# Performance work log

Measured on AMD Instinct MI355X. Metric: run time of the kernel, lower is better.

Reference implementation:

```python
import jax, jax.numpy as jnp
import numpy as np

# --- static configuration (mirrors PMETorchPME(alpha=1.0, mesh=1.0), interpolation_nodes=6) ---
ALPHA = 1.0            # Gaussian smearing sigma of CoulombPotential
MESH_SPACING = 1.0
BOX_L = 120.0
NS = (120, 120, 120)   # ceil(BOX_L / MESH_SPACING) per axis; static for jit
ORDER = 6              # interpolation nodes (6-point stencil per axis)
N_ATOMS = 100000
PI = np.pi


def _interp_weights(x):
    # x: (N,3) offsets in [-0.5, 0.5) relative to the midpoint of the 6-point stencil.
    # Lagrange interpolation on nodes t_j = j - 2.5, j = 0..5 (even-order, midpoint-centered).
    t = np.arange(ORDER) - (ORDER - 1) / 2.0                 # (6,) node positions
    diff = x[..., None] - jnp.asarray(t, x.dtype)            # (N,3,6)
    ws = []
    for j in range(ORDER):
        idx = [k for k in range(ORDER) if k != j]
        denom = float(np.prod([t[j] - t[k] for k in idx]))
        ws.append(jnp.prod(diff[..., idx], axis=-1) / denom)
    return jnp.stack(ws, axis=-1)                            # (N,3,6)


def _stencil(coords, box):
    # Map positions to mesh units, build per-particle 6x6x6 stencil weights + flat mesh indices.
    frac = coords @ jnp.linalg.inv(box)                      # fractional coordinates
    pos = frac * jnp.asarray(NS, coords.dtype)               # (N,3) in mesh units
    i0 = jnp.floor(pos)
    x = pos - (i0 + 0.5)                                     # offset from stencil midpoint
    w = _interp_weights(x)                                   # (N,3,6)
    offs = jnp.arange(ORDER, dtype=jnp.int32) - (ORDER // 2 - 1)   # [-2..3]
    ns_i = jnp.asarray(NS, jnp.int32)
    g = (i0.astype(jnp.int32)[..., None] + offs) % ns_i[None, :, None]  # (N,3,6) periodic
    W = w[:, 0, :, None, None] * w[:, 1, None, :, None] * w[:, 2, None, None, :]   # (N,6,6,6)
    flat = (g[:, 0, :, None, None] * NS[1] + g[:, 1, None, :, None]) * NS[2] + g[:, 2, None, None, :]
    n = coords.shape[0]
    return W.reshape(n, -1), flat.reshape(n, -1)             # (N,216) each


def _kspace_kernel(box, dtype):
    # G(k) = 4*pi * exp(-sigma^2 k^2 / 2) / k^2, zero at k=0 (CoulombPotential.lr_from_k_sq)
    inv_cell = jnp.linalg.inv(box)
    m0 = jnp.fft.fftfreq(NS[0]) * NS[0]
    m1 = jnp.fft.fftfreq(NS[1]) * NS[1]
    m2 = jnp.fft.rfftfreq(NS[2]) * NS[2]
    m = jnp.stack(jnp.meshgrid(m0, m1, m2, indexing="ij"), axis=-1).astype(dtype)
    k = 2.0 * PI * jnp.einsum("xyzm,nm->xyzn", m, inv_cell)  # k = 2*pi * inv(cell) @ m
    k_sq = jnp.sum(k * k, axis=-1)
    safe = jnp.where(k_sq > 0, k_sq, 1.0)
    return jnp.where(k_sq > 0, 4.0 * PI * jnp.exp(-0.5 * ALPHA * ALPHA * k_sq) / safe, 0.0)


def setup_inputs() -> dict:
    key = jax.random.key(0)
    k1, k2 = jax.random.split(key)
    coords = jax.random.uniform(k1, (N_ATOMS, 3), dtype=jnp.float32) * BOX_L
    box = (BOX_L * jnp.eye(3, dtype=jnp.float32))
    charges = jax.random.normal(k2, (N_ATOMS, 1), dtype=jnp.float32)
    return {"coords": coords, "box": box, "charges": charges}


def reference(coords, box, charges):
    q = charges[:, 0]                                        # (N,)
    W, flat = _stencil(coords, box)                          # (N,216)
    ntot = NS[0] * NS[1] * NS[2]
    # charge spreading (scatter-add)
    mesh = jnp.zeros((ntot,), coords.dtype).at[flat.reshape(-1)].add((W * q[:, None]).reshape(-1))
    mesh = mesh.reshape(NS)
    # FFT convolution with the reciprocal-space Coulomb kernel
    G = _kspace_kernel(box, coords.dtype)
    pot_mesh = jnp.fft.irfftn(jnp.fft.rfftn(mesh, norm="backward") * G, s=NS, norm="forward")
    # gather back to particles
    pot = jnp.sum(pot_mesh.reshape(-1)[flat] * W, axis=-1)   # (N,)
    volume = jnp.abs(jnp.linalg.det(box))
    pot = pot / volume
    pot = pot - q * (np.sqrt(2.0 / PI) / ALPHA)              # remove self-contribution
    pot = pot - 2.0 * (PI * ALPHA * ALPHA) * jnp.sum(q) / volume  # charge-neutral background
    pot = pot / 2.0
    return jnp.sum(q * pot)                                  # energy = sum(charges * potentials)
```

## Files before the change

kernel.cpp:

```cpp
#include <hip/hip_runtime.h>
#include <math.h>

#define NMESH 120
#define NKZ 61
#define ALPHA_C 1.0

#define TILE 12
#define NTPD 10
#define NTILE 1000
#define FP 17
#define ZPAD 20
#define FPSTRIDE 5792
#define CAP 256

#define CHUNK 128
#define WXA_OFF 0
#define WYA_OFF (CHUNK*ZPAD)
#define WZA_OFF (2*CHUNK*ZPAD)
#define LYS_OFF (3*CHUNK*ZPAD)
#define SMEMF   (LYS_OFF + CHUNK)

#define YCH 12
#define XCH 4
#define YROW 137

#define NSLOT 64
#define SLOTSTRIDE 8
#define W120C (-0.052359877559829887f)

typedef float v2f __attribute__((ext_vector_type(2)));

#define EK_OFF      0
#define Q_OFF       4096
#define Q2_OFF      8192
#define COUNTS_OFF  12288
#define BUF_OFF     115264
#define C1_OFF      23283264
#define C2_OFF      115264
#define SORTED_OFF  (C1_OFF + 4096)

__device__ inline void inv3(const float* b, float* ib) {
    float a00=b[0],a01=b[1],a02=b[2],a10=b[3],a11=b[4],a12=b[5],a20=b[6],a21=b[7],a22=b[8];
    float c00 =  a11*a22 - a12*a21;
    float c01 = -(a10*a22 - a12*a20);
    float c02 =  a10*a21 - a11*a20;
    float c10 = -(a01*a22 - a02*a21);
    float c11 =  a00*a22 - a02*a20;
    float c12 = -(a00*a21 - a01*a20);
    float c20 =  a01*a12 - a02*a11;
    float c21 = -(a00*a12 - a02*a10);
    float c22 =  a00*a11 - a01*a10;
    float det = a00*c00 + a01*c01 + a02*c02;
    float inv = 1.0f/det;
    ib[0]=c00*inv; ib[1]=c10*inv; ib[2]=c20*inv;
    ib[3]=c01*inv; ib[4]=c11*inv; ib[5]=c21*inv;
    ib[6]=c02*inv; ib[7]=c12*inv; ib[8]=c22*inv;
}

__device__ inline void atom_pos(const float* __restrict__ box, float c0, float c1, float c2,
                                float* p) {
    float ib[9]; inv3(box, ib);
    #pragma unroll
    for (int d=0; d<3; ++d)
        p[d] = (c0*ib[0+d] + c1*ib[3+d] + c2*ib[6+d]) * 120.0f;
}

__device__ inline int wrap120(int i) { return ((i % 120) + 120) % 120; }

__device__ inline void lag6(float x, float* w) {
    float df[6];
    #pragma unroll
    for (int k=0;k<6;++k) df[k] = x - ((float)k - 2.5f);
    w[0] = df[1]*df[2]*df[3]*df[4]*df[5] * (-1.0f/120.0f);
    w[1] = df[0]*df[2]*df[3]*df[4]*df[5] * ( 1.0f/24.0f);
    w[2] = df[0]*df[1]*df[3]*df[4]*df[5] * (-1.0f/12.0f);
    w[3] = df[0]*df[1]*df[2]*df[4]*df[5] * ( 1.0f/12.0f);
    w[4] = df[0]*df[1]*df[2]*df[3]*df[5] * (-1.0f/24.0f);
    w[5] = df[0]*df[1]*df[2]*df[3]*df[4] * ( 1.0f/120.0f);
}

__device__ inline int halo_pairs(int c, int* t, int* l) {
    int r = c % 12, ti = c / 12, n = 0;
    t[n] = ti;          l[n] = r + 2;  n++;
    if (r < 3)  { t[n] = (ti+9)%10; l[n] = r + 14; n++; }
    if (r >= 10){ t[n] = (ti+1)%10; l[n] = r - 10; n++; }
    return n;
}

__device__ inline void dft8(const float2* xin, float2* Y) {
    const float S = 0.70710678118654752f;
    float2 a=xin[0], b=xin[2], c=xin[4], d=xin[6];
    float s02r=a.x+c.x, s02i=a.y+c.y, d02r=a.x-c.x, d02i=a.y-c.y;
    float s13r=b.x+d.x, s13i=b.y+d.y, d13r=b.x-d.x, d13i=b.y-d.y;
    float2 E0 = make_float2(s02r+s13r, s02i+s13i);
    float2 E1 = make_float2(d02r+d13i, d02i-d13r);
    float2 E2 = make_float2(s02r-s13r, s02i-s13i);
    float2 E3 = make_float2(d02r-d13i, d02i+d13r);
    a=xin[1]; b=xin[3]; c=xin[5]; d=xin[7];
    s02r=a.x+c.x; s02i=a.y+c.y; d02r=a.x-c.x; d02i=a.y-c.y;
    s13r=b.x+d.x; s13i=b.y+d.y; d13r=b.x-d.x; d13i=b.y-d.y;
    float2 O0 = make_float2(s02r+s13r, s02i+s13i);
    float2 O1 = make_float2(d02r+d13i, d02i-d13r);
    float2 O2 = make_float2(s02r-s13r, s02i-s13i);
    float2 O3 = make_float2(d02r-d13i, d02i+d13r);
    float t1r = S*(O1.x + O1.y), t1i = S*(O1.y - O1.x);
    float t2r = O2.y,            t2i = -O2.x;
    float t3r = S*(O3.y - O3.x), t3i = -S*(O3.x + O3.y);
    Y[0] = make_float2(E0.x + O0.x, E0.y + O0.y);
    Y[4] = make_float2(E0.x - O0.x, E0.y - O0.y);
    Y[1] = make_float2(E1.x + t1r,  E1.y + t1i);
    Y[5] = make_float2(E1.x - t1r,  E1.y - t1i);
    Y[2] = make_float2(E2.x + t2r,  E2.y + t2i);
    Y[6] = make_float2(E2.x - t2r,  E2.y - t2i);
    Y[3] = make_float2(E3.x + t3r,  E3.y + t3i);
    Y[7] = make_float2(E3.x - t3r,  E3.y - t3i);
}

__global__ void scatter_q_kernel(const float* __restrict__ coords,
                                 const float* __restrict__ box,
                                 const float* __restrict__ charges,
                                 int* __restrict__ counts,
                                 float4* __restrict__ sorted,
                                 double* __restrict__ qslots,
                                 double* __restrict__ q2slots, int n) {
    int i = blockIdx.x*blockDim.x + threadIdx.x;
    float v = 0.f, v2 = 0.f;
    if (i < n) {
        float p[3]; atom_pos(box, coords[3*i], coords[3*i+1], coords[3*i+2], p);
        float q = charges[i];
        v = q; v2 = q*q;
        int t[3];
        #pragma unroll
        for (int d=0; d<3; ++d) t[d] = wrap120((int)floorf(p[d])) / TILE;
        int tile = (t[0]*NTPD + t[1])*NTPD + t[2];
        int idx = atomicAdd(&counts[tile], 1);
        if (idx < CAP) sorted[tile*CAP + idx] = make_float4(p[0], p[1], p[2], q);
    }
    #pragma unroll
    for (int o=32;o>0;o>>=1) { v += __shfl_down(v,o,64); v2 += __shfl_down(v2,o,64); }
    __shared__ float s1[4], s2[4];
    int lane = threadIdx.x & 63, w = threadIdx.x >> 6;
    if (lane==0) { s1[w]=v; s2[w]=v2; }
    __syncthreads();
    if (threadIdx.x==0) {
        for (int j=1;j<4;j++) { v += s1[j]; v2 += s2[j]; }
        int slot = (blockIdx.x & (NSLOT-1)) * SLOTSTRIDE;
        atomicAdd(&qslots[slot],  (double)v);
        atomicAdd(&q2slots[slot], (double)v2);
    }
}

__global__ void __launch_bounds__(256, 4)
spread_tile_kernel(const float4* __restrict__ sorted,
                   const int* __restrict__ counts,
                   float* __restrict__ buf) {
    int tile = blockIdx.x;
    int tx = tile / (NTPD*NTPD);
    int rem = tile - tx*NTPD*NTPD;
    int ty = rem / NTPD;
    int tz = rem - ty*NTPD;
    int bx = tx*TILE, by = ty*TILE, bz = tz*TILE;

    __shared__ float smem[SMEMF];
    int* lys = (int*)&smem[LYS_OFF];

    int tid  = threadIdx.x;
    int wv   = tid >> 6;
    int lane = tid & 63;
    int half = wv & 1;
    int blo  = (wv < 2) ? 0 : 9;
    int t3   = lane / 17; if (t3 > 2) t3 = 2;
    int A    = lane - 17*t3; if (A > 16) A = 16;
    bool owner = (lane < 51);
    int B0   = blo + 3*t3;
    bool c2ok = (B0 + 2 <= 16);

    v2f   acc2[3][8];
    float acc16[3];
    #pragma unroll
    for (int c=0;c<3;++c) {
        #pragma unroll
        for (int k=0;k<8;++k) acc2[c][k] = (v2f){0.f,0.f};
        acc16[c] = 0.f;
    }

    int cntT = min(counts[tile], CAP);
    const float4* src = sorted + (size_t)tile*CAP;

    for (int start = 0; start < cntT; start += CHUNK) {
        int jn = cntT - start; if (jn > CHUNK) jn = CHUNK;
        __syncthreads();
        if (tid < jn) {
            float4 s = src[start + tid];
            float fx = floorf(s.x), fy = floorf(s.y), fz = floorf(s.z);
            float wx[6]; lag6(s.x - (fx + 0.5f), wx);
            float wy[6]; lag6(s.y - (fy + 0.5f), wy);
            float wz[6]; lag6(s.z - (fz + 0.5f), wz);
            int lx = wrap120((int)fx) - bx;
            int ly = wrap120((int)fy) - by;
            int lz = wrap120((int)fz) - bz;
            float4 z4 = make_float4(0.f,0.f,0.f,0.f);
            float4* px = (float4*)&smem[WXA_OFF + tid*ZPAD];
            float4* py = (float4*)&smem[WYA_OFF + tid*ZPAD];
            float4* pz = (float4*)&smem[WZA_OFF + tid*ZPAD];
            #pragma unroll
            for (int k=0;k<5;++k) { px[k]=z4; py[k]=z4; pz[k]=z4; }
            #pragma unroll
            for (int k=0;k<6;++k) {
                smem[WXA_OFF + tid*ZPAD + lx + k] = wx[k];
                smem[WYA_OFF + tid*ZPAD + ly + k] = wy[k];
                smem[WZA_OFF + tid*ZPAD + lz + k] = wz[k]*s.w;
            }
            lys[tid] = ly;
        }
        __syncthreads();
        int idxA = lane, idxB = 64 + lane;
        int lyA = lys[idxA], lyB = lys[idxB];
        bool rA = blo ? (lyA >= 4) : (lyA <= 8);
        bool rB = blo ? (lyB >= 4) : (lyB <= 8);
        bool gA = (idxA < jn) && rA && ((idxA & 1) == half);
        bool gB = (idxB < jn) && rB && ((idxB & 1) == half);
        unsigned long long mA = __ballot(gA);
        unsigned long long mB = __ballot(gB);
        auto body = [&](int j) {
            float wx_ = smem[WXA_OFF + j*ZPAD + A];
            float wy0 = smem[WYA_OFF + j*ZPAD + B0];
            float wy1 = smem[WYA_OFF + j*ZPAD + B0 + 1];
            float wy2 = smem[WYA_OFF + j*ZPAD + B0 + 2];
            float w2c[3];
            w2c[0] = wx_*wy0;
            w2c[1] = wx_*wy1;
            w2c[2] = c2ok ? wx_*wy2 : 0.f;
            const float4* zp = (const float4*)&smem[WZA_OFF + j*ZPAD];
            float4 z0 = zp[0], z1 = zp[1], z2 = zp[2], z3 = zp[3];
            float z16 = smem[WZA_OFF + j*ZPAD + 16];
            v2f zz[8];
            zz[0]=(v2f){z0.x,z0.y}; zz[1]=(v2f){z0.z,z0.w};
            zz[2]=(v2f){z1.x,z1.y}; zz[3]=(v2f){z1.z,z1.w};
            zz[4]=(v2f){z2.x,z2.y}; zz[5]=(v2f){z2.z,z2.w};
            zz[6]=(v2f){z3.x,z3.y}; zz[7]=(v2f){z3.z,z3.w};
            #pragma unroll
            for (int c=0;c<3;++c) {
                v2f wv2 = (v2f){w2c[c], w2c[c]};
                #pragma unroll
                for (int k=0;k<8;++k) acc2[c][k] += wv2 * zz[k];
                acc16[c] = fmaf(w2c[c], z16, acc16[c]);
            }
        };
        while (mA) { int j = __builtin_ctzll(mA); mA &= mA - 1ull; body(j); }
        while (mB) { int j = 64 + __builtin_ctzll(mB); mB &= mB - 1ull; body(j); }
    }
    __syncthreads();
    if ((half == 0) && owner) {
        #pragma unroll
        for (int c=0;c<3;++c) {
            int Bc = B0 + c;
            if (Bc <= 16) {
                float* dst = &smem[(A*17 + Bc)*ZPAD];
                *(float4*)&dst[0]  = make_float4(acc2[c][0].x, acc2[c][0].y, acc2[c][1].x, acc2[c][1].y);
                *(float4*)&dst[4]  = make_float4(acc2[c][2].x, acc2[c][2].y, acc2[c][3].x, acc2[c][3].y);
                *(float4*)&dst[8]  = make_float4(acc2[c][4].x, acc2[c][4].y, acc2[c][5].x, acc2[c][5].y);
                *(float4*)&dst[12] = make_float4(acc2[c][6].x, acc2[c][6].y, acc2[c][7].x, acc2[c][7].y);
                dst[16] = acc16[c];
            }
        }
    }
    __syncthreads();
    if ((half == 1) && owner) {
        #pragma unroll
        for (int c=0;c<3;++c) {
            int Bc = B0 + c;
            if (Bc <= 16) {
                float* dst = &smem[(A*17 + Bc)*ZPAD];
                float4 a0 = *(float4*)&dst[0],  a1 = *(float4*)&dst[4];
                float4 a2 = *(float4*)&dst[8],  a3 = *(float4*)&dst[12];
                float  a4 = dst[16];
                *(float4*)&dst[0]  = make_float4(a0.x+acc2[c][0].x, a0.y+acc2[c][0].y, a0.z+acc2[c][1].x, a0.w+acc2[c][1].y);
                *(float4*)&dst[4]  = make_float4(a1.x+acc2[c][2].x, a1.y+acc2[c][2].y, a1.z+acc2[c][3].x, a1.w+acc2[c][3].y);
                *(float4*)&dst[8]  = make_float4(a2.x+acc2[c][4].x, a2.y+acc2[c][4].y, a2.z+acc2[c][5].x, a2.w+acc2[c][5].y);
                *(float4*)&dst[12] = make_float4(a3.x+acc2[c][6].x, a3.y+acc2[c][6].y, a3.z+acc2[c][7].x, a3.w+acc2[c][7].y);
                dst[16] = a4 + acc16[c];
            }
        }
    }
    __syncthreads();
    float4* bp = (float4*)(buf + (size_t)tile * FPSTRIDE);
    const float4* sp = (const float4*)smem;
    for (int i = tid; i < FPSTRIDE/4; i += 256) bp[i] = sp[i];
}

#define DFT15_BODY(Yp, kfreq, RE, IM)                                        \
    float w1r = tw[kfreq].x, w1i = tw[kfreq].y;                              \
    float w2r = w1r*w1r - w1i*w1i, w2i = 2.f*w1r*w1i;                        \
    float w3r = w2r*w1r - w2i*w1i, w3i = w2r*w1i + w2i*w1r;                  \
    float ar=1.f, ai=0.f, br=w1r, bi=w1i, cr=w2r, ci=w2i;                    \
    float r0_=0.f,i0_=0.f,r1_=0.f,i1_=0.f,r2_=0.f,i2_=0.f;                   \
    _Pragma("unroll")                                                        \
    for (int s_=0;s_<5;++s_) {                                               \
        float2 ya = (Yp)[3*s_], yb = (Yp)[3*s_+1], yc = (Yp)[3*s_+2];        \
        r0_ = fmaf(ya.x, ar, fmaf(-ya.y, ai, r0_));                          \
        i0_ = fmaf(ya.x, ai, fmaf( ya.y, ar, i0_));                          \
        r1_ = fmaf(yb.x, br, fmaf(-yb.y, bi, r1_));                          \
        i1_ = fmaf(yb.x, bi, fmaf( yb.y, br, i1_));                          \
        r2_ = fmaf(yc.x, cr, fmaf(-yc.y, ci, r2_));                          \
        i2_ = fmaf(yc.x, ci, fmaf( yc.y, cr, i2_));                          \
        float n_;                                                            \
        n_ = ar*w3r - ai*w3i; ai = ar*w3i + ai*w3r; ar = n_;                 \
        n_ = br*w3r - bi*w3i; bi = br*w3i + bi*w3r; br = n_;                 \
        n_ = cr*w3r - ci*w3i; ci = cr*w3i + ci*w3r; cr = n_;                 \
    }                                                                        \
    float RE = (r0_+r1_)+r2_, IM = (i0_+i1_)+i2_;

#define TWIDDLE_INIT()                                                       \
    __shared__ float2 tw[120];                                               \
    for (int k_ = threadIdx.x; k_ < 120; k_ += blockDim.x) {                 \
        float s_, c_; __sincosf(W120C * (float)k_, &s_, &c_);                \
        tw[k_] = make_float2(c_, s_);                                        \
    }

__global__ void __launch_bounds__(256)
fft_z_kernel(const float* __restrict__ buf,
             float2* __restrict__ C1) {
    int x  = blockIdx.x / 10;
    int y0 = (blockIdx.x - x*10) * YCH;
    __shared__ float  lin[YCH][121];
    __shared__ float2 Ys[YCH][YROW];
    TWIDDLE_INIT()

    int txA[2], lxA[2];
    int nx = halo_pairs(x, txA, lxA);

    for (int i = threadIdx.x; i < YCH*120; i += 256) {
        int yl = i / 120, z = i - yl*120;
        int tyA[2], lyA[2]; int ny = halo_pairs(y0 + yl, tyA, lyA);
        int tzA[2], lzA[2]; int nz = halo_pairs(z, tzA, lzA);
        float s = 0.f;
        for (int ii=0; ii<nx; ++ii)
            for (int jj=0; jj<ny; ++jj)
                for (int kk=0; kk<nz; ++kk) {
                    int tile = (txA[ii]*NTPD + tyA[jj])*NTPD + tzA[kk];
                    int cell = (lxA[ii]*FP + lyA[jj])*ZPAD + lzA[kk];
                    s += buf[(size_t)tile*FPSTRIDE + cell];
                }
        lin[yl][z] = s;
    }
    __syncthreads();
    for (int t = threadIdx.x; t < YCH*15; t += 256) {
        int yl = t / 15, j = t - (t/15)*15;
        float2 xin[8], Yo[8];
        #pragma unroll
        for (int m=0;m<8;++m) xin[m] = make_float2(lin[yl][15*m+j], 0.f);
        dft8(xin, Yo);
        #pragma unroll
        for (int r=0;r<8;++r) Ys[yl][r*17+j] = Yo[r];
    }
    __syncthreads();
    for (int o = threadIdx.x; o < YCH*NKZ; o += 256) {
        int kz = o / YCH, yl = o - (o/YCH)*YCH;
        const float2* Yp = &Ys[yl][(kz&7)*17];
        DFT15_BODY(Yp, kz, re, im)
        C1[(x*NKZ + kz)*120 + y0 + yl] = make_float2(re, im);
    }
}

__global__ void __launch_bounds__(256)
fft_y_kernel(const float2* __restrict__ C1,
             float2* __restrict__ C2) {
    int xc = blockIdx.x / NKZ;
    int kz = blockIdx.x - xc*NKZ;
    int x0 = xc * XCH;
    __shared__ float2 lin[XCH][121];
    __shared__ float2 Ys[XCH][YROW];
    TWIDDLE_INIT()
    for (int i = threadIdx.x; i < XCH*120; i += 256) {
        int xo = i / 120, y = i - (i/120)*120;
        lin[xo][y] = C1[((x0+xo)*NKZ + kz)*120 + y];
    }
    __syncthreads();
    for (int t = threadIdx.x; t < XCH*15; t += 256) {
        int xo = t / 15, j = t - (t/15)*15;
        float2 xin[8], Yo[8];
        #pragma unroll
        for (int m=0;m<8;++m) xin[m] = lin[xo][15*m+j];
        dft8(xin, Yo);
        #pragma unroll
        for (int r=0;r<8;++r) Ys[xo][r*17+j] = Yo[r];
    }
    __syncthreads();
    for (int o = threadIdx.x; o < XCH*120; o += 256) {
        int ky = o >> 2, xo = o & 3;
        const float2* Yp = &Ys[xo][(ky&7)*17];
        DFT15_BODY(Yp, ky, re, im)
        C2[(kz*120 + ky)*120 + x0 + xo] = make_float2(re, im);
    }
}

__global__ void __launch_bounds__(256)
fft_x_energy_kernel(const float2* __restrict__ C2,
                    const float* __restrict__ box,
                    double* __restrict__ ekslots) {
    int kyc = blockIdx.x / NKZ;
    int kz  = blockIdx.x - kyc*NKZ;
    int ky0 = kyc * XCH;
    __shared__ float2 lin[XCH][121];
    __shared__ float2 Ys[XCH][YROW];
    TWIDDLE_INIT()
    const float2* src = C2 + (kz*120 + ky0)*120;
    for (int i = threadIdx.x; i < XCH*120; i += 256) {
        int kyo = i / 120, xx = i - (i/120)*120;
        lin[kyo][xx] = src[i];
    }
    __syncthreads();
    for (int t = threadIdx.x; t < XCH*15; t += 256) {
        int kyo = t / 15, j = t - (t/15)*15;
        float2 xin[8], Yo[8];
        #pragma unroll
        for (int m=0;m<8;++m) xin[m] = lin[kyo][15*m+j];
        dft8(xin, Yo);
        #pragma unroll
        for (int r=0;r<8;++r) Ys[kyo][r*17+j] = Yo[r];
    }
    __syncthreads();
    float ib[9]; inv3(box, ib);
    const float TWOPI = 6.283185307179586f;
    float wzf = (kz==0 || kz==60) ? 1.0f : 2.0f;
    float contrib = 0.f;
    for (int o = threadIdx.x; o < XCH*120; o += 256) {
        int kyo = o / 120, kx = o - (o/120)*120;
        int ky = ky0 + kyo;
        const float2* Yp = &Ys[kyo][(kx&7)*17];
        DFT15_BODY(Yp, kx, re, im)
        if (!(kx==0 && ky==0 && kz==0)) {
            float mx = (kx < 60) ? (float)kx : (float)(kx - 120);
            float my = (ky < 60) ? (float)ky : (float)(ky - 120);
            float mz = (float)kz;
            float k0 = TWOPI*(mx*ib[0] + my*ib[1] + mz*ib[2]);
            float k1 = TWOPI*(mx*ib[3] + my*ib[4] + mz*ib[5]);
            float k2 = TWOPI*(mx*ib[6] + my*ib[7] + mz*ib[8]);
            float ksq = k0*k0 + k1*k1 + k2*k2;
            float G = 12.566370614359172f * __expf(-0.5f*(float)(ALPHA_C*ALPHA_C)*ksq) / ksq;
            contrib += wzf * G * (re*re + im*im);
        }
    }
    #pragma unroll
    for (int o=32;o>0;o>>=1) contrib += __shfl_down(contrib,o,64);
    __shared__ float sm[4];
    int lane = threadIdx.x & 63, w = threadIdx.x >> 6;
    if (lane==0) sm[w] = contrib;
    __syncthreads();
    if (threadIdx.x==0)
        atomicAdd(&ekslots[(blockIdx.x & (NSLOT-1)) * SLOTSTRIDE],
                  (double)(sm[0]+sm[1]+sm[2]+sm[3]));
}

__global__ void finalize_kernel(const double* __restrict__ ekslots,
                                const double* __restrict__ qslots,
                                const double* __restrict__ q2slots,
                                const float* __restrict__ box,
                                float* __restrict__ out) {
    int lane = threadIdx.x;
    double ek  = ekslots[lane*SLOTSTRIDE];
    double sq  = qslots [lane*SLOTSTRIDE];
    double sq2 = q2slots[lane*SLOTSTRIDE];
    #pragma unroll
    for (int o=32;o>0;o>>=1) {
        ek  += __shfl_down(ek,  o, 64);
        sq  += __shfl_down(sq,  o, 64);
        sq2 += __shfl_down(sq2, o, 64);
    }
    if (lane == 0) {
        double a00=box[0],a01=box[1],a02=box[2],a10=box[3],a11=box[4],a12=box[5],a20=box[6],a21=box[7],a22=box[8];
        double det = a00*(a11*a22-a12*a21) - a01*(a10*a22-a12*a20) + a02*(a10*a21-a11*a20);
        double vol = fabs(det);
        double E = ek/(2.0*vol)
                 - 0.5*sqrt(2.0/M_PI)/ALPHA_C * sq2
                 - M_PI*ALPHA_C*ALPHA_C * sq*sq / vol;
        out[0] = (float)E;
    }
}

extern "C" void kernel_launch(void* const* d_in, const int* in_sizes, int n_in,
                              void* d_out, int out_size, void* d_ws, size_t ws_size,
                              hipStream_t stream) {
    const float* coords  = (const float*)d_in[0];
    const float* box     = (const float*)d_in[1];
    const float* charges = (const float*)d_in[2];
    int n = in_sizes[0] / 3;

    char* ws = (char*)d_ws;
    double* ekslots = (double*)(ws + EK_OFF);
    double* qslots  = (double*)(ws + Q_OFF);
    double* q2slots = (double*)(ws + Q2_OFF);
    float*  buf     = (float*) (ws + BUF_OFF);
    float2* C1      = (float2*)(ws + C1_OFF);
    float2* C2      = (float2*)(ws + C2_OFF);
    int* counts     = (int*)(ws + COUNTS_OFF);
    float4* sorted  = (float4*)(ws + SORTED_OFF);

    int gA = (n + 255)/256;
    hipMemsetAsync(ws, 0, 16384, stream);
    scatter_q_kernel<<<gA, 256, 0, stream>>>(coords, box, charges, counts, sorted, qslots, q2slots, n);
    spread_tile_kernel<<<NTILE, 256, 0, stream>>>(sorted, counts, buf);
    fft_z_kernel<<<120*10, 256, 0, stream>>>(buf, C1);
    fft_y_kernel<<<30*NKZ, 256, 0, stream>>>(C1, C2);
    fft_x_energy_kernel<<<NKZ*30, 256, 0, stream>>>(C2, box, ekslots);
    finalize_kernel<<<1, 64, 0, stream>>>(ekslots, qslots, q2slots, box, (float*)d_out);
}
```

Baseline: 146.7 us.

## Skip empty z-segments in spread accumulation and widen FFT y/x chunking

In the tile spreading kernel, each particle's z-offset within the tile is stored in shared memory and broadcast with readlane. The code then updates only the float4 segments of the z accumulator that can hold nonzero weights, which avoids FMAs on zero-padded entries. Separately, XCH grows from 4 to 8, so each y/x FFT block handles twice as many columns and half as many blocks are launched. The branches are wave-uniform, but the XCH change halves the grid and raises shared memory per block, which may lower occupancy.

New measurement: 146.7 us. About the same (-0.0%).

```diff
diff --git a/kernel.cpp b/kernel.cpp
--- a/kernel.cpp
+++ b/kernel.cpp
@@ -18,10 +18,11 @@
 #define WYA_OFF (CHUNK*ZPAD)
 #define WZA_OFF (2*CHUNK*ZPAD)
 #define LYS_OFF (3*CHUNK*ZPAD)
-#define SMEMF   (LYS_OFF + CHUNK)
+#define LZS_OFF (LYS_OFF + CHUNK)
+#define SMEMF   (LZS_OFF + CHUNK)
 
 #define YCH 12
-#define XCH 4
+#define XCH 8
 #define YROW 137
 
 #define NSLOT 64
@@ -163,6 +164,7 @@
 
     __shared__ float smem[SMEMF];
     int* lys = (int*)&smem[LYS_OFF];
+    int* lzs = (int*)&smem[LZS_OFF];
 
     int tid  = threadIdx.x;
     int wv   = tid >> 6;
@@ -212,17 +214,19 @@
                 smem[WZA_OFF + tid*ZPAD + lz + k] = wz[k]*s.w;
             }
             lys[tid] = ly;
+            lzs[tid] = lz;
         }
         __syncthreads();
         int idxA = lane, idxB = 64 + lane;
         int lyA = lys[idxA], lyB = lys[idxB];
+        int lzAv = lzs[idxA], lzBv = lzs[idxB];
         bool rA = blo ? (lyA >= 4) : (lyA <= 8);
         bool rB = blo ? (lyB >= 4) : (lyB <= 8);
         bool gA = (idxA < jn) && rA && ((idxA & 1) == half);
         bool gB = (idxB < jn) && rB && ((idxB & 1) == half);
         unsigned long long mA = __ballot(gA);
         unsigned long long mB = __ballot(gB);
-        auto body = [&](int j) {
+        auto body = [&](int j, int lzj) {
             float wx_ = smem[WXA_OFF + j*ZPAD + A];
             float wy0 = smem[WYA_OFF + j*ZPAD + B0];
             float wy1 = smem[WYA_OFF + j*ZPAD + B0 + 1];
@@ -232,23 +236,56 @@
             w2c[1] = wx_*wy1;
             w2c[2] = c2ok ? wx_*wy2 : 0.f;
             const float4* zp = (const float4*)&smem[WZA_OFF + j*ZPAD];
-            float4 z0 = zp[0], z1 = zp[1], z2 = zp[2], z3 = zp[3];
-            float z16 = smem[WZA_OFF + j*ZPAD + 16];
-            v2f zz[8];
-            zz[0]=(v2f){z0.x,z0.y}; zz[1]=(v2f){z0.z,z0.w};
-            zz[2]=(v2f){z1.x,z1.y}; zz[3]=(v2f){z1.z,z1.w};
-            zz[4]=(v2f){z2.x,z2.y}; zz[5]=(v2f){z2.z,z2.w};
-            zz[6]=(v2f){z3.x,z3.y}; zz[7]=(v2f){z3.z,z3.w};
-            #pragma unroll
-            for (int c=0;c<3;++c) {
-                v2f wv2 = (v2f){w2c[c], w2c[c]};
+            if (lzj <= 3) {
+                float4 z0 = zp[0];
                 #pragma unroll
-                for (int k=0;k<8;++k) acc2[c][k] += wv2 * zz[k];
-                acc16[c] = fmaf(w2c[c], z16, acc16[c]);
+                for (int c=0;c<3;++c) {
+                    v2f wv2 = (v2f){w2c[c], w2c[c]};
+                    acc2[c][0] += wv2 * (v2f){z0.x, z0.y};
+                    acc2[c][1] += wv2 * (v2f){z0.z, z0.w};
+                }
+            }
+            if (lzj <= 7) {
+                float4 z1 = zp[1];
+                #pragma unroll
+                for (int c=0;c<3;++c) {
+                    v2f wv2 = (v2f){w2c[c], w2c[c]};
+                    acc2[c][2] += wv2 * (v2f){z1.x, z1.y};
+                    acc2[c][3] += wv2 * (v2f){z1.z, z1.w};
+                }
+            }
+            if (lzj >= 3) {
+                float4 z2 = zp[2];
+                #pragma unroll
+                for (int c=0;c<3;++c) {
+                    v2f wv2 = (v2f){w2c[c], w2c[c]};
+                    acc2[c][4] += wv2 * (v2f){z2.x, z2.y};
+                    acc2[c][5] += wv2 * (v2f){z2.z, z2.w};
+                }
+            }
+            if (lzj >= 7) {
+                float4 z3 = zp[3];
+                #pragma unroll
+                for (int c=0;c<3;++c) {
+                    v2f wv2 = (v2f){w2c[c], w2c[c]};
+                    acc2[c][6] += wv2 * (v2f){z3.x, z3.y};
+                    acc2[c][7] += wv2 * (v2f){z3.z, z3.w};
+                }
+            }
+            if (lzj == 11) {
+                float z16 = smem[WZA_OFF + j*ZPAD + 16];
+                #pragma unroll
+                for (int c=0;c<3;++c) acc16[c] = fmaf(w2c[c], z16, acc16[c]);
             }
         };
-        while (mA) { int j = __builtin_ctzll(mA); mA &= mA - 1ull; body(j); }
-        while (mB) { int j = 64 + __builtin_ctzll(mB); mB &= mB - 1ull; body(j); }
+        while (mA) {
+            int j = __builtin_ctzll(mA); mA &= mA - 1ull;
+            body(j, __builtin_amdgcn_readlane(lzAv, j));
+        }
+        while (mB) {
+            int jj = __builtin_ctzll(mB); mB &= mB - 1ull;
+            body(64 + jj, __builtin_amdgcn_readlane(lzBv, jj));
+        }
     }
     __syncthreads();
     if ((half == 0) && owner) {
@@ -388,7 +425,7 @@
     }
     __syncthreads();
     for (int o = threadIdx.x; o < XCH*120; o += 256) {
-        int ky = o >> 2, xo = o & 3;
+        int ky = o >> 3, xo = o & 7;
         const float2* Yp = &Ys[xo][(ky&7)*17];
         DFT15_BODY(Yp, ky, re, im)
         C2[(kz*120 + ky)*120 + x0 + xo] = make_float2(re, im);
@@ -502,7 +539,7 @@
     scatter_q_kernel<<<gA, 256, 0, stream>>>(coords, box, charges, counts, sorted, qslots, q2slots, n);
     spread_tile_kernel<<<NTILE, 256, 0, stream>>>(sorted, counts, buf);
     fft_z_kernel<<<120*10, 256, 0, stream>>>(buf, C1);
-    fft_y_kernel<<<30*NKZ, 256, 0, stream>>>(C1, C2);
-    fft_x_energy_kernel<<<NKZ*30, 256, 0, stream>>>(C2, box, ekslots);
+    fft_y_kernel<<<15*NKZ, 256, 0, stream>>>(C1, C2);
+    fft_x_energy_kernel<<<NKZ*15, 256, 0, stream>>>(C2, box, ekslots);
     finalize_kernel<<<1, 64, 0, stream>>>(ekslots, qslots, q2slots, box, (float*)d_out);
 }
```
